# Kernel optimization log

Hardware: AMD Instinct MI355X
Metric: run time of the kernel (lower is better)

## Reference

```python
import jax, jax.numpy as jnp
import numpy as np

N, X_DIM, Y_DIM, HID = 8192, 512, 2048 // 4, 2048
Y_DIM = 512

def setup_inputs() -> dict:
    key = jax.random.key(0)
    ks = jax.random.split(key, 10)
    def lin(k, fan_in, fan_out):
        lim = 1.0 / np.sqrt(fan_in)
        kw, kb = jax.random.split(k)
        W = jax.random.uniform(kw, (fan_in, fan_out), jnp.float32, -lim, lim)
        b = jax.random.uniform(kb, (fan_out,), jnp.float32, -lim, lim)
        return W, b
    mu_W1, mu_b1 = lin(ks[0], X_DIM, HID)
    mu_W2, mu_b2 = lin(ks[1], HID, Y_DIM)
    lv_W1, lv_b1 = lin(ks[2], X_DIM, HID)
    lv_W2, lv_b2 = lin(ks[3], HID, Y_DIM)
    return {
        "x_samples": jax.random.normal(ks[4], (N, X_DIM), jnp.float32),
        "y_samples": jax.random.normal(ks[5], (N, Y_DIM), jnp.float32),
        "mu_W1": mu_W1, "mu_b1": mu_b1, "mu_W2": mu_W2, "mu_b2": mu_b2,
        "lv_W1": lv_W1, "lv_b1": lv_b1, "lv_W2": lv_W2, "lv_b2": lv_b2,
    }

def reference(x_samples, y_samples, mu_W1, mu_b1, mu_W2, mu_b2, lv_W1, lv_b1, lv_W2, lv_b2):
    # MLP heads (GEMMs)
    mu = jax.nn.relu(x_samples @ mu_W1 + mu_b1) @ mu_W2 + mu_b2          # [N, D]
    logvar = jnp.tanh(jax.nn.relu(x_samples @ lv_W1 + lv_b1) @ lv_W2 + lv_b2)  # [N, D]
    w = 0.5 * jnp.exp(-logvar)                                           # 1/(2*exp(logvar))
    n = x_samples.shape[0]

    # positive: -mean_i sum_d (mu_id - y_id)^2 * w_id
    positive = -(((mu - y_samples) ** 2) * w).sum(axis=1).mean()

    # negative (exact decomposition of the [N,N,D] broadcast):
    # -(1/N^2) sum_{i,d} w_id * (N*mu_id^2 - 2*mu_id*Sy_d + Sy2_d)
    Sy = y_samples.sum(axis=0)          # [D]
    Sy2 = (y_samples ** 2).sum(axis=0)  # [D]
    negative = -(w * (n * mu ** 2 - 2.0 * mu * Sy + Sy2)).sum() / (n * n)

    return positive - negative
```

## Files before the change

kernel.cpp:

```cpp
#include <hip/hip_runtime.h>
#include <hip/hip_bf16.h>
#include <stdint.h>

#define NS   8192
#define XD   512
#define HD   2048
#define YD   512

typedef unsigned short u16;
using bf16x8 = __attribute__((ext_vector_type(8))) short;
using f32x4  = __attribute__((ext_vector_type(4))) float;

__device__ __forceinline__ float bf2f(u16 u) {
  union { uint32_t i; float f; } v; v.i = ((uint32_t)u) << 16; return v.f;
}
__device__ __forceinline__ u16 f2b(float f) {
  __hip_bfloat16 hb = __float2bfloat16(f);
  return *(const u16*)&hb;
}
__device__ __forceinline__ float ld_in(const void* p, int f32, size_t i) {
  return f32 ? ((const float*)p)[i] : bf2f(((const u16*)p)[i]);
}
#define GLDS(gp, lp) __builtin_amdgcn_global_load_lds( \
    (__attribute__((address_space(1))) void*)(gp),     \
    (__attribute__((address_space(3))) void*)(lp), 16, 0, 0)

__device__ __forceinline__ int probe_f32(const void* p, int n_u16, int* sflag) {
  if (threadIdx.x == 0) *sflag = 0;
  __syncthreads();
  const u16* q = (const u16*)p;
  int wild = 0;
  for (int i = threadIdx.x; i < n_u16; i += blockDim.x) {
    float v = bf2f(q[i]);
    if (!(fabsf(v) <= 1000.0f)) wild = 1;
  }
  if (wild) *sflag = 1;
  __syncthreads();
  int r = *sflag;
  __syncthreads();
  return r;
}

__global__ __launch_bounds__(256) void prep_all(
    const void* __restrict__ x,
    const void* w1m, const void* b1m, const void* w2m, const void* b2m,
    const void* w1l, const void* b1l, const void* w2l, const void* b2l,
    const void* __restrict__ y,
    u16* __restrict__ xb, float* __restrict__ biasv,
    u16* __restrict__ W1t, u16* __restrict__ W2tm, u16* __restrict__ W2tl,
    float* __restrict__ Sy, float* __restrict__ Sy2) {
  __shared__ u16 tile[64 * 72];
  __shared__ int sflag;
  const int b = blockIdx.x;
  const int tid = threadIdx.x;

  if (b < 2048) {
    if (!probe_f32(x, 1024, &sflag)) return;
    const size_t base = (size_t)b * 2048 + (size_t)tid * 8;
    alignas(16) u16 o[8];
    const float4* s = (const float4*)((const float*)x + base);
    float4 v0 = s[0], v1 = s[1];
    o[0]=f2b(v0.x); o[1]=f2b(v0.y); o[2]=f2b(v0.z); o[3]=f2b(v0.w);
    o[4]=f2b(v1.x); o[5]=f2b(v1.y); o[6]=f2b(v1.z); o[7]=f2b(v1.w);
    *(uint4*)(xb + base) = *(const uint4*)o;
  } else if (b == 2048) {
    const int f3 = probe_f32(b1m, 1024, &sflag);
    const int f5 = probe_f32(b2m, 512, &sflag);
    const int f7 = probe_f32(b1l, 1024, &sflag);
    const int f9 = probe_f32(b2l, 512, &sflag);
    for (int i = tid; i < 5120; i += 256) {
      float v;
      if (i < 2048)      v = ld_in(b1m, f3, i);
      else if (i < 4096) v = ld_in(b1l, f7, i - 2048);
      else if (i < 4608) v = ld_in(b2m, f5, i - 4096);
      else               v = ld_in(b2l, f9, i - 4608);
      biasv[i] = v;
    }
  } else if (b < 3073) {
    const int id = b - 2049, which = id >> 8, t = id & 255;
    const void* in; u16* out; int R, C;
    if (which == 0)      { in = w1m; out = W1t;                   R = XD; C = HD; }
    else if (which == 1) { in = w2m; out = W2tm;                  R = HD; C = YD; }
    else if (which == 2) { in = w1l; out = W1t + (size_t)HD * XD; R = XD; C = HD; }
    else                 { in = w2l; out = W2tl;                  R = HD; C = YD; }
    const int f = probe_f32(in, 1024, &sflag);
    const int nbx = C >> 6;
    const int c0 = (t % nbx) * 64, r0 = (t / nbx) * 64;
    const int r = tid >> 2, cc = (tid & 3) * 16;
    if (f) {
      const float4* s = (const float4*)((const float*)in + (size_t)(r0 + r) * C + c0 + cc);
#pragma unroll
      for (int k = 0; k < 4; ++k) {
        float4 v = s[k];
        tile[r * 72 + cc + k * 4 + 0] = f2b(v.x);
        tile[r * 72 + cc + k * 4 + 1] = f2b(v.y);
        tile[r * 72 + cc + k * 4 + 2] = f2b(v.z);
        tile[r * 72 + cc + k * 4 + 3] = f2b(v.w);
      }
    } else {
      const uint4* s = (const uint4*)((const u16*)in + (size_t)(r0 + r) * C + c0 + cc);
      *(uint4*)&tile[r * 72 + cc]     = s[0];
      *(uint4*)&tile[r * 72 + cc + 8] = s[1];
    }
    __syncthreads();
    const int i = tid >> 2, jc = (tid & 3) * 16;
    alignas(16) u16 o[16];
#pragma unroll
    for (int j = 0; j < 16; ++j) o[j] = tile[(jc + j) * 72 + i];
    uint4* dq = (uint4*)&out[(size_t)(c0 + i) * R + r0 + jc];
    dq[0] = ((const uint4*)o)[0];
    dq[1] = ((const uint4*)o)[1];
  } else {
    const int id2 = b - 3073;
    const int yf = probe_f32(y, 1024, &sflag);
    const int half = tid >> 7;
    const int c0 = (tid & 127) * 4;
    const int r0 = id2 * 128 + half * 64;
    float s0 = 0.f, s1 = 0.f, s2 = 0.f, s3 = 0.f;
    float q0 = 0.f, q1 = 0.f, q2 = 0.f, q3 = 0.f;
    for (int r = r0; r < r0 + 64; r += 4) {
#pragma unroll
      for (int rr = 0; rr < 4; ++rr) {
        float v0, v1, v2, v3;
        if (yf) {
          const float4 t4 = *(const float4*)((const float*)y + (size_t)(r + rr) * YD + c0);
          v0 = t4.x; v1 = t4.y; v2 = t4.z; v3 = t4.w;
        } else {
          const uint2 t2 = *(const uint2*)((const u16*)y + (size_t)(r + rr) * YD + c0);
          v0 = bf2f((u16)(t2.x & 0xffff)); v1 = bf2f((u16)(t2.x >> 16));
          v2 = bf2f((u16)(t2.y & 0xffff)); v3 = bf2f((u16)(t2.y >> 16));
        }
        s0 += v0; q0 += v0 * v0;  s1 += v1; q1 += v1 * v1;
        s2 += v2; q2 += v2 * v2;  s3 += v3; q3 += v3 * v3;
      }
    }
    atomicAdd(&Sy[c0],     s0);  atomicAdd(&Sy2[c0],     q0);
    atomicAdd(&Sy[c0 + 1], s1);  atomicAdd(&Sy2[c0 + 1], q1);
    atomicAdd(&Sy[c0 + 2], s2);  atomicAdd(&Sy2[c0 + 2], q2);
    atomicAdd(&Sy[c0 + 3], s3);  atomicAdd(&Sy2[c0 + 3], q3);
  }
}

#define SYNC_PRE do { \
  __builtin_amdgcn_sched_barrier(0); \
  __builtin_amdgcn_s_barrier(); \
  asm volatile("s_waitcnt lgkmcnt(0)" ::: "memory"); \
  __builtin_amdgcn_sched_barrier(0); \
  __builtin_amdgcn_s_setprio(1); } while (0)
#define SYNC_POST do { \
  __builtin_amdgcn_s_setprio(0); \
  __builtin_amdgcn_sched_barrier(0); \
  __builtin_amdgcn_s_barrier(); \
  __builtin_amdgcn_sched_barrier(0); } while (0)
#define VMCNT(N) asm volatile("s_waitcnt vmcnt(" #N ")" ::: "memory")
#define SCB __builtin_amdgcn_sched_barrier(0)

#define RD_A(MH, BUF) do { \
  const u16* ab_ = &lds[((BUF)*2 + wm) * 8192]; \
  _Pragma("unroll") for (int q_ = 0; q_ < 4; ++q_) \
    _Pragma("unroll") for (int ks_ = 0; ks_ < 2; ++ks_) \
      af[q_][ks_] = *(const bf16x8*)&ab_[((MH)*64 + q_*16 + c16)*64 + (((ks_*4+quad) ^ cswz) << 3)]; \
} while (0)

#define RD_B(NH, BUF) do { \
  const u16* bb_ = &lds[32768 + ((BUF)*2 + (wn>>1)) * 8192]; \
  _Pragma("unroll") for (int p_ = 0; p_ < 2; ++p_) \
    _Pragma("unroll") for (int ks_ = 0; ks_ < 2; ++ks_) \
      bf[(NH)*2+p_][ks_] = *(const bf16x8*)&bb_[((wn&1)*64 + ((NH)*2+p_)*16 + c16)*64 + (((ks_*4+quad) ^ cswz) << 3)]; \
} while (0)

#define MM(MH, NH) do { \
  _Pragma("unroll") for (int ks_ = 0; ks_ < 2; ++ks_) \
    _Pragma("unroll") for (int q_ = 0; q_ < 4; ++q_) \
      _Pragma("unroll") for (int p_ = 0; p_ < 2; ++p_) \
        acc[(MH)*4+q_][(NH)*2+p_] = __builtin_amdgcn_mfma_f32_16x16x32_bf16( \
            af[q_][ks_], bf[(NH)*2+p_][ks_], acc[(MH)*4+q_][(NH)*2+p_], 0, 0, 0); \
} while (0)

#define ST_A(KT, HALF) do { if ((KT) < 8) { \
  u16* lb_ = &lds[(((KT)&1)*2 + (HALF))*8192 + (wid << 9)]; \
  const u16* sp_ = Aptr + (size_t)(bm0 + (HALF)*128 + (wid<<3) + srow)*512 + ((KT)<<6) + scg; \
  GLDS(sp_, lb_); GLDS(sp_ + (size_t)64*512, lb_ + 4096); } } while (0)

#define ST_B(KT, HALF) do { if ((KT) < 8) { \
  u16* lb_ = &lds[32768 + (((KT)&1)*2 + (HALF))*8192 + (wid << 9)]; \
  const u16* sp_ = W1t + (size_t)(bn0 + (HALF)*128 + (wid<<3) + srow)*512 + ((KT)<<6) + scg; \
  GLDS(sp_, lb_); GLDS(sp_ + (size_t)64*512, lb_ + 4096); } } while (0)

__global__ __launch_bounds__(512, 2) void gemm1_kernel(
    const void* __restrict__ xraw, const u16* __restrict__ xb,
    const u16* __restrict__ W1t,
    const float* __restrict__ bias,
    u16* __restrict__ h_mu, u16* __restrict__ h_lv) {
  __shared__ alignas(16) u16 lds[65536];
  __shared__ int sflag;
  const int tid = threadIdx.x;

  const u16* Aptr = probe_f32(xraw, 1024, &sflag) ? xb : (const u16*)xraw;

  const int wid = tid >> 6, lane = tid & 63;
  const int wm = wid >> 2, wn = wid & 3;
  const int quad = lane >> 4, c16 = lane & 15, cswz = c16 & 7;
  const int srow = lane >> 3;
  const int scg  = ((lane & 7) ^ srow) << 3;

  const int id = blockIdx.x;
  const int xcd = id & 7, slot = id >> 3;
  const int bm0 = (xcd * 4 + (slot & 3)) * 256;
  const int bn0 = (slot >> 2) * 256;

  f32x4 acc[8][4] = {};
  bf16x8 af[4][2], bf[4][2];

  ST_B(0, 0); ST_B(0, 1); ST_A(0, 0); ST_A(0, 1);
  ST_B(1, 0); ST_B(1, 1);
  VMCNT(4);
  __builtin_amdgcn_s_barrier();
  __builtin_amdgcn_sched_barrier(0);

#pragma unroll
  for (int i = 0; i < 4; ++i) {
    const int ka = 2 * i, kb = ka + 1;
    const bool last = (i == 3);
    RD_A(0, 0); RD_B(0, 0); ST_A(kb, 0);
    SYNC_PRE; MM(0, 0); SYNC_POST;
    RD_B(1, 0); ST_A(kb, 1);
    SYNC_PRE; MM(0, 1); SYNC_POST;
    RD_A(1, 0); ST_B(ka + 2, 0);
    SYNC_PRE; MM(1, 0); SYNC_POST;
    ST_B(ka + 2, 1);
    SYNC_PRE; MM(1, 1);
    if (!last) { VMCNT(4); } else { VMCNT(0); }
    SYNC_POST;
    RD_A(0, 1); RD_B(0, 1); ST_A(ka + 2, 0);
    SYNC_PRE; MM(0, 0); SYNC_POST;
    RD_B(1, 1); ST_A(ka + 2, 1);
    SYNC_PRE; MM(0, 1); SYNC_POST;
    RD_A(1, 1); ST_B(kb + 2, 0);
    SYNC_PRE; MM(1, 0); SYNC_POST;
    ST_B(kb + 2, 1);
    SYNC_PRE; MM(1, 1);
    if (!last) { VMCNT(4); }
    SYNC_POST;
  }

  u16* myl = &lds[wid * 8192];
  const bool is_lv = bn0 >= HD;
  u16* dst = is_lv ? h_lv : h_mu;
  const int wncol = wn << 6;
  const int gc0 = (bn0 - (is_lv ? HD : 0)) + wncol;
  const int grow0 = bm0 + (wm << 7);
#pragma unroll
  for (int ni = 0; ni < 4; ++ni) {
    const float bv = bias[bn0 + wncol + ni * 16 + c16];
#pragma unroll
    for (int mi = 0; mi < 8; ++mi)
#pragma unroll
      for (int r = 0; r < 4; ++r) {
        const int row = mi * 16 + (quad << 2) + r;
        const int col = ni * 16 + c16;
        myl[row * 64 + ((((col >> 3) ^ (row & 7)) << 3) | (col & 7))] =
            f2b(fmaxf(acc[mi][ni][r] + bv, 0.f));
      }
  }
#pragma unroll
  for (int it = 0; it < 16; ++it) {
    const int row = (it << 3) + (lane >> 3);
    const int ch = lane & 7;
    const uint4 v = *(const uint4*)&myl[row * 64 + ((ch ^ (row & 7)) << 3)];
    *(uint4*)&dst[(size_t)(grow0 + row) * HD + gc0 + (ch << 3)] = v;
  }
}

#undef RD_A
#undef RD_B
#undef MM
#undef ST_A
#undef ST_B

#define LDA8(AF, T) do { \
  const uint64_t o_ = (uint64_t)(T) * 128u; \
  asm volatile("global_load_dwordx4 %0, %1, off"           : "=v"(AF[0][0]) : "v"(aA[0] + o_)); \
  asm volatile("global_load_dwordx4 %0, %1, off offset:64" : "=v"(AF[0][1]) : "v"(aA[0] + o_)); \
  asm volatile("global_load_dwordx4 %0, %1, off"           : "=v"(AF[1][0]) : "v"(aA[1] + o_)); \
  asm volatile("global_load_dwordx4 %0, %1, off offset:64" : "=v"(AF[1][1]) : "v"(aA[1] + o_)); \
  asm volatile("global_load_dwordx4 %0, %1, off"           : "=v"(AF[2][0]) : "v"(aA[2] + o_)); \
  asm volatile("global_load_dwordx4 %0, %1, off offset:64" : "=v"(AF[2][1]) : "v"(aA[2] + o_)); \
  asm volatile("global_load_dwordx4 %0, %1, off"           : "=v"(AF[3][0]) : "v"(aA[3] + o_)); \
  asm volatile("global_load_dwordx4 %0, %1, off offset:64" : "=v"(AF[3][1]) : "v"(aA[3] + o_)); \
} while (0)

#define RD8(BF, BUFI) do { \
  _Pragma("unroll") for (int ni_ = 0; ni_ < 4; ++ni_) \
    _Pragma("unroll") for (int ks_ = 0; ks_ < 2; ++ks_) \
      BF[ni_][ks_] = *(const bf16x8*)&lds[(BUFI)*16384 + rbase + \
          (wn*64 + ni_*16 + c16)*64 + (((ks_*4+quad) ^ cswz) << 3)]; \
} while (0)

#define MM32(AF, BF) do { \
  _Pragma("unroll") for (int ks_ = 0; ks_ < 2; ++ks_) \
    _Pragma("unroll") for (int mi_ = 0; mi_ < 4; ++mi_) \
      _Pragma("unroll") for (int ni_ = 0; ni_ < 4; ++ni_) \
        acc[mi_][ni_] = __builtin_amdgcn_mfma_f32_16x16x32_bf16( \
            AF[mi_][ks_], BF[ni_][ks_], acc[mi_][ni_], 0, 0, 0); \
} while (0)

#define STB2(KT) do { \
  u16* lbm_ = lds + ((KT)&3)*16384 + (wid << 9); \
  const u16* spm_ = bMp + (size_t)(KT)*64; \
  GLDS(spm_, lbm_); GLDS(spm_ + (size_t)64*HD, lbm_ + 4096); \
  u16* lbl_ = lds + ((KT)&3)*16384 + 8192 + (wid << 9); \
  const u16* spl_ = bLp + (size_t)(KT)*64; \
  GLDS(spl_, lbl_); GLDS(spl_ + (size_t)64*HD, lbl_ + 4096); \
} while (0)

#define PH2(T, AFc, AFn, BFc, BFn) do { \
  SCB; LDA8(AFn, (T) + 1); SCB; STB2((T) + 2); SCB; \
  VMCNT(12); SCB; \
  __builtin_amdgcn_s_barrier(); SCB; \
  RD8(BFn, ((T) + 1) & 3); \
  __builtin_amdgcn_s_setprio(1); \
  MM32(AFc, BFc); \
  __builtin_amdgcn_s_setprio(0); \
} while (0)

__global__ __launch_bounds__(512, 1) void gemm2_dual(
    const u16* __restrict__ hm, const u16* __restrict__ hl,
    const u16* __restrict__ W2m, const u16* __restrict__ W2l,
    const float* __restrict__ b2m, const float* __restrict__ b2l,
    const void* __restrict__ y,
    const float* __restrict__ Sy, const float* __restrict__ Sy2,
    double* __restrict__ gacc, unsigned* __restrict__ counter,
    float* __restrict__ out) {
  __shared__ alignas(16) u16 lds[65536];
  __shared__ double bs[8];
  __shared__ int sflag;

  const int yf = probe_f32(y, 1024, &sflag);

  const int tid = threadIdx.x, wid = tid >> 6, lane = tid & 63;
  const int wh = wid >> 2;
  const int wm = (wid >> 1) & 1, wn = wid & 1;
  const int quad = lane >> 4, c16 = lane & 15, cswz = c16 & 7;
  const int srow = lane >> 3;
  const int scg  = ((lane & 7) ^ srow) << 3;
  const int rbase = wh * 8192;

  const int id = blockIdx.x;
  const int xcd = id & 7, slot = id >> 3;
  const int bm0 = (xcd * 8 + (slot >> 2)) * 128;
  const int bn0 = (slot & 3) * 128;

  const u16* bMp = W2m + (size_t)(bn0 + (wid << 3) + srow) * HD + scg;
  const u16* bLp = W2l + (size_t)(bn0 + (wid << 3) + srow) * HD + scg;

  const u16* hx = wh ? hl : hm;
  uint64_t aA[4];
#pragma unroll
  for (int mi = 0; mi < 4; ++mi)
    aA[mi] = (uint64_t)(uintptr_t)(
        hx + (size_t)(bm0 + wm * 64 + mi * 16 + c16) * HD + quad * 8);

  f32x4 acc[4][4] = {};
  bf16x8 afA[4][2], afB[4][2], bfA[4][2], bfB[4][2];

  STB2(0); STB2(1);
  SCB;
  LDA8(afA, 0);
  SCB;
  VMCNT(12);
  __builtin_amdgcn_s_barrier();
  SCB;
  RD8(bfA, 0);

#pragma unroll 1
  for (int i = 0; i < 28; i += 4) {
    PH2(i + 0, afA, afB, bfA, bfB);
    PH2(i + 1, afB, afA, bfB, bfA);
    PH2(i + 2, afA, afB, bfA, bfB);
    PH2(i + 3, afB, afA, bfB, bfA);
  }
  PH2(28, afA, afB, bfA, bfB);
  PH2(29, afB, afA, bfB, bfA);
  SCB; LDA8(afB, 31); SCB;
  VMCNT(8);
  SCB;
  __builtin_amdgcn_s_barrier();
  SCB;
  RD8(bfB, 3);
  __builtin_amdgcn_s_setprio(1);
  MM32(afA, bfA);
  __builtin_amdgcn_s_setprio(0);
  SCB;
  VMCNT(0);
  SCB;
  __builtin_amdgcn_s_setprio(1);
  MM32(afB, bfB);
  __builtin_amdgcn_s_setprio(0);

  __syncthreads();
  float* ldsF = (float*)lds;
  float* mur = ldsF + (wid & 3) * 4224;
  if (wh == 0) {
#pragma unroll
    for (int ni = 0; ni < 4; ++ni) {
      const float bmv = b2m[bn0 + wn * 64 + ni * 16 + c16];
#pragma unroll
      for (int mi = 0; mi < 4; ++mi)
#pragma unroll
        for (int r = 0; r < 4; ++r)
          mur[(mi * 16 + quad * 4 + r) * 66 + ni * 16 + c16] =
              acc[mi][ni][r] + bmv;
    }
  }
  __syncthreads();
  const float invN = 1.0f / (float)NS;
  float s = 0.f;
  if (wh == 1) {
#pragma unroll
    for (int ni = 0; ni < 4; ++ni) {
      const int gcol = bn0 + wn * 64 + ni * 16 + c16;
      const float blv = b2l[gcol];
      const float syv = Sy[gcol], sy2v = Sy2[gcol];
#pragma unroll
      for (int mi = 0; mi < 4; ++mi)
#pragma unroll
        for (int r = 0; r < 4; ++r) {
          const int grow = bm0 + wm * 64 + mi * 16 + quad * 4 + r;
          const float m   = mur[(mi * 16 + quad * 4 + r) * 66 + ni * 16 + c16];
          const float lvp = acc[mi][ni][r] + blv;
          const float w   = 0.5f * expf(-tanhf(lvp));
          const float yv  = ld_in(y, yf, (size_t)grow * YD + gcol);
          s += w * (yv * yv - 2.f * m * yv + (2.f * m * syv - sy2v) * invN);
        }
    }
  }
  for (int off = 32; off > 0; off >>= 1) s += __shfl_down(s, off);
  if (lane == 0) bs[wid] = (double)s;
  __syncthreads();
  if (tid == 0) {
    atomicAdd(gacc, bs[0] + bs[1] + bs[2] + bs[3] +
                    bs[4] + bs[5] + bs[6] + bs[7]);
    __threadfence();
    const unsigned old = atomicAdd(counter, 1u);
    if (old == gridDim.x - 1) {
      const double g = atomicAdd(gacc, 0.0);
      out[0] = (float)(-g / (double)NS);
    }
  }
}

extern "C" void kernel_launch(void* const* d_in, const int* in_sizes, int n_in,
                              void* d_out, int out_size, void* d_ws, size_t ws_size,
                              hipStream_t stream) {
  char* ws = (char*)d_ws;
  double*   gacc    = (double*)ws;
  unsigned* counter = (unsigned*)(ws + 8);
  float*    Sy      = (float*)(ws + 128);
  float*    Sy2     = (float*)(ws + 2176);
  float*    biasv   = (float*)(ws + 4224);
  u16* xb   = (u16*)(ws + 24704);
  u16* W1t  = xb + (size_t)NS * XD;
  u16* W2tm = W1t + (size_t)2 * HD * XD;
  u16* W2tl = W2tm + (size_t)YD * HD;
  u16* h_mu = W2tl + (size_t)YD * HD;
  u16* h_lv = h_mu + (size_t)NS * HD;

  hipMemsetAsync(d_ws, 0, 4224, stream);

  prep_all<<<2049 + 1024 + 64, 256, 0, stream>>>(
      d_in[0], d_in[2], d_in[3], d_in[4], d_in[5],
      d_in[6], d_in[7], d_in[8], d_in[9], d_in[1],
      xb, biasv, W1t, W2tm, W2tl, Sy, Sy2);

  const float* b1  = biasv;
  const float* b2m = biasv + 4096, *b2l = biasv + 4608;

  gemm1_kernel<<<(NS / 256) * ((2 * HD) / 256), 512, 0, stream>>>(
      d_in[0], xb, W1t, b1, h_mu, h_lv);

  gemm2_dual<<<(NS / 128) * (YD / 128), 512, 0, stream>>>(
      h_mu, h_lv, W2tm, W2tl, b2m, b2l, d_in[1], Sy, Sy2,
      gacc, counter, (float*)d_out);
}
```

Measured before the change: 262.6 us.

## Shrink gemm2 B ring to three LDS stages and allow two blocks per CU

Reduces the W2 LDS ring from four stages to three and drops the double-buffered B fragment registers in favour of a single set read at the start of each phase. It then raises launch bounds to two blocks per CU, which is meant to let a second block hide latency. The cost is that the B LDS read is no longer overlapped with the previous phase's MFMAs, because each phase now waits on lgkmcnt before computing. Register pressure under the tighter launch bound may also cause spills.

After: 261.4 us. No clear change (-0.5%).

```diff
diff --git a/kernel.cpp b/kernel.cpp
--- a/kernel.cpp
+++ b/kernel.cpp
@@ -153,6 +153,7 @@
   __builtin_amdgcn_s_barrier(); \
   __builtin_amdgcn_sched_barrier(0); } while (0)
 #define VMCNT(N) asm volatile("s_waitcnt vmcnt(" #N ")" ::: "memory")
+#define LGKM0 asm volatile("s_waitcnt lgkmcnt(0)" ::: "memory")
 #define SCB __builtin_amdgcn_sched_barrier(0)
 
 #define RD_A(MH, BUF) do { \
@@ -290,41 +291,43 @@
   asm volatile("global_load_dwordx4 %0, %1, off offset:64" : "=v"(AF[3][1]) : "v"(aA[3] + o_)); \
 } while (0)
 
-#define RD8(BF, BUFI) do { \
+#define RD8(BUFI) do { \
   _Pragma("unroll") for (int ni_ = 0; ni_ < 4; ++ni_) \
     _Pragma("unroll") for (int ks_ = 0; ks_ < 2; ++ks_) \
-      BF[ni_][ks_] = *(const bf16x8*)&lds[(BUFI)*16384 + rbase + \
+      bf[ni_][ks_] = *(const bf16x8*)&lds[(BUFI)*16384 + rbase + \
           (wn*64 + ni_*16 + c16)*64 + (((ks_*4+quad) ^ cswz) << 3)]; \
 } while (0)
 
-#define MM32(AF, BF) do { \
+#define MM32(AF) do { \
   _Pragma("unroll") for (int ks_ = 0; ks_ < 2; ++ks_) \
     _Pragma("unroll") for (int mi_ = 0; mi_ < 4; ++mi_) \
       _Pragma("unroll") for (int ni_ = 0; ni_ < 4; ++ni_) \
         acc[mi_][ni_] = __builtin_amdgcn_mfma_f32_16x16x32_bf16( \
-            AF[mi_][ks_], BF[ni_][ks_], acc[mi_][ni_], 0, 0, 0); \
-} while (0)
-
-#define STB2(KT) do { \
-  u16* lbm_ = lds + ((KT)&3)*16384 + (wid << 9); \
+            AF[mi_][ks_], bf[ni_][ks_], acc[mi_][ni_], 0, 0, 0); \
+} while (0)
+
+#define STB2(KT, BI) do { \
+  u16* lbm_ = lds + (BI)*16384 + (wid << 9); \
   const u16* spm_ = bMp + (size_t)(KT)*64; \
   GLDS(spm_, lbm_); GLDS(spm_ + (size_t)64*HD, lbm_ + 4096); \
-  u16* lbl_ = lds + ((KT)&3)*16384 + 8192 + (wid << 9); \
+  u16* lbl_ = lbm_ + 8192; \
   const u16* spl_ = bLp + (size_t)(KT)*64; \
   GLDS(spl_, lbl_); GLDS(spl_ + (size_t)64*HD, lbl_ + 4096); \
 } while (0)
 
-#define PH2(T, AFc, AFn, BFc, BFn) do { \
-  SCB; LDA8(AFn, (T) + 1); SCB; STB2((T) + 2); SCB; \
+#define PH6(T, AFc, AFn, BR, BS) do { \
+  SCB; RD8(BR); SCB; \
+  LDA8(AFn, (T) + 1); SCB; \
+  STB2((T) + 2, BS); SCB; \
+  LGKM0; SCB; \
   VMCNT(12); SCB; \
   __builtin_amdgcn_s_barrier(); SCB; \
-  RD8(BFn, ((T) + 1) & 3); \
   __builtin_amdgcn_s_setprio(1); \
-  MM32(AFc, BFc); \
-  __builtin_amdgcn_s_setprio(0); \
-} while (0)
-
-__global__ __launch_bounds__(512, 1) void gemm2_dual(
+  MM32(AFc); \
+  __builtin_amdgcn_s_setprio(0); SCB; \
+} while (0)
+
+__global__ __launch_bounds__(512, 2) void gemm2_dual(
     const u16* __restrict__ hm, const u16* __restrict__ hl,
     const u16* __restrict__ W2m, const u16* __restrict__ W2l,
     const float* __restrict__ b2m, const float* __restrict__ b2l,
@@ -332,7 +335,7 @@
     const float* __restrict__ Sy, const float* __restrict__ Sy2,
     double* __restrict__ gacc, unsigned* __restrict__ counter,
     float* __restrict__ out) {
-  __shared__ alignas(16) u16 lds[65536];
+  __shared__ alignas(16) u16 lds[49152];
   __shared__ double bs[8];
   __shared__ int sflag;
 
@@ -362,40 +365,40 @@
         hx + (size_t)(bm0 + wm * 64 + mi * 16 + c16) * HD + quad * 8);
 
   f32x4 acc[4][4] = {};
-  bf16x8 afA[4][2], afB[4][2], bfA[4][2], bfB[4][2];
-
-  STB2(0); STB2(1);
+  bf16x8 afA[4][2], afB[4][2], bf[4][2];
+
+  STB2(0, 0); STB2(1, 1);
   SCB;
   LDA8(afA, 0);
   SCB;
   VMCNT(12);
   __builtin_amdgcn_s_barrier();
   SCB;
-  RD8(bfA, 0);
 
 #pragma unroll 1
-  for (int i = 0; i < 28; i += 4) {
-    PH2(i + 0, afA, afB, bfA, bfB);
-    PH2(i + 1, afB, afA, bfB, bfA);
-    PH2(i + 2, afA, afB, bfA, bfB);
-    PH2(i + 3, afB, afA, bfB, bfA);
-  }
-  PH2(28, afA, afB, bfA, bfB);
-  PH2(29, afB, afA, bfB, bfA);
-  SCB; LDA8(afB, 31); SCB;
+  for (int i = 0; i < 5; ++i) {
+    PH6(6 * i + 0, afA, afB, 0, 2);
+    PH6(6 * i + 1, afB, afA, 1, 0);
+    PH6(6 * i + 2, afA, afB, 2, 1);
+    PH6(6 * i + 3, afB, afA, 0, 2);
+    PH6(6 * i + 4, afA, afB, 1, 0);
+    PH6(6 * i + 5, afB, afA, 2, 1);
+  }
+  SCB; RD8(0); SCB;
+  LDA8(afB, 31); SCB;
+  LGKM0; SCB;
   VMCNT(8);
   SCB;
-  __builtin_amdgcn_s_barrier();
-  SCB;
-  RD8(bfB, 3);
+  __builtin_amdgcn_s_barrier(); SCB;
   __builtin_amdgcn_s_setprio(1);
-  MM32(afA, bfA);
-  __builtin_amdgcn_s_setprio(0);
-  SCB;
+  MM32(afA);
+  __builtin_amdgcn_s_setprio(0); SCB;
+  RD8(1); SCB;
+  LGKM0; SCB;
   VMCNT(0);
   SCB;
   __builtin_amdgcn_s_setprio(1);
-  MM32(afB, bfB);
+  MM32(afB);
   __builtin_amdgcn_s_setprio(0);
 
   __syncthreads();
```

## Stage A tiles through LDS with double buffering and run two blocks per CU

Applied to the files above, without the earlier changes.

The second-GEMM kernel stops loading A fragments straight from global memory into registers. A and B tiles are now both staged into LDS via global_load_lds using a two-buffer ping-pong (32K elements per buffer), and each step waits for all loads with a full vmcnt(0). Only one set of fragment registers remains, and launch bounds go from 1 to 2 blocks per CU so two workgroups can overlap each other's latency. The trade-off is a shallower per-block prefetch (one tile ahead instead of two) and extra LDS traffic for A, in exchange for fewer registers and more occupancy.

Measured after the change: 236.5 us. -9.9%, faster.

```diff
diff --git a/kernel.cpp b/kernel.cpp
--- a/kernel.cpp
+++ b/kernel.cpp
@@ -278,53 +278,49 @@
 #undef ST_A
 #undef ST_B
 
-#define LDA8(AF, T) do { \
-  const uint64_t o_ = (uint64_t)(T) * 128u; \
-  asm volatile("global_load_dwordx4 %0, %1, off"           : "=v"(AF[0][0]) : "v"(aA[0] + o_)); \
-  asm volatile("global_load_dwordx4 %0, %1, off offset:64" : "=v"(AF[0][1]) : "v"(aA[0] + o_)); \
-  asm volatile("global_load_dwordx4 %0, %1, off"           : "=v"(AF[1][0]) : "v"(aA[1] + o_)); \
-  asm volatile("global_load_dwordx4 %0, %1, off offset:64" : "=v"(AF[1][1]) : "v"(aA[1] + o_)); \
-  asm volatile("global_load_dwordx4 %0, %1, off"           : "=v"(AF[2][0]) : "v"(aA[2] + o_)); \
-  asm volatile("global_load_dwordx4 %0, %1, off offset:64" : "=v"(AF[2][1]) : "v"(aA[2] + o_)); \
-  asm volatile("global_load_dwordx4 %0, %1, off"           : "=v"(AF[3][0]) : "v"(aA[3] + o_)); \
-  asm volatile("global_load_dwordx4 %0, %1, off offset:64" : "=v"(AF[3][1]) : "v"(aA[3] + o_)); \
-} while (0)
-
-#define RD8(BF, BUFI) do { \
+#define RDA8(BUF) do { \
+  _Pragma("unroll") for (int mi_ = 0; mi_ < 4; ++mi_) \
+    _Pragma("unroll") for (int ks_ = 0; ks_ < 2; ++ks_) \
+      af[mi_][ks_] = *(const bf16x8*)&lds[(BUF)*32768 + abase + \
+          (wm*64 + mi_*16 + c16)*64 + (((ks_*4+quad) ^ cswz) << 3)]; \
+} while (0)
+
+#define RDB8(BUF) do { \
   _Pragma("unroll") for (int ni_ = 0; ni_ < 4; ++ni_) \
     _Pragma("unroll") for (int ks_ = 0; ks_ < 2; ++ks_) \
-      BF[ni_][ks_] = *(const bf16x8*)&lds[(BUFI)*16384 + rbase + \
+      bf[ni_][ks_] = *(const bf16x8*)&lds[(BUF)*32768 + bbase + \
           (wn*64 + ni_*16 + c16)*64 + (((ks_*4+quad) ^ cswz) << 3)]; \
 } while (0)
 
-#define MM32(AF, BF) do { \
+#define MM32 do { \
   _Pragma("unroll") for (int ks_ = 0; ks_ < 2; ++ks_) \
     _Pragma("unroll") for (int mi_ = 0; mi_ < 4; ++mi_) \
       _Pragma("unroll") for (int ni_ = 0; ni_ < 4; ++ni_) \
         acc[mi_][ni_] = __builtin_amdgcn_mfma_f32_16x16x32_bf16( \
-            AF[mi_][ks_], BF[ni_][ks_], acc[mi_][ni_], 0, 0, 0); \
-} while (0)
-
-#define STB2(KT) do { \
-  u16* lbm_ = lds + ((KT)&3)*16384 + (wid << 9); \
-  const u16* spm_ = bMp + (size_t)(KT)*64; \
-  GLDS(spm_, lbm_); GLDS(spm_ + (size_t)64*HD, lbm_ + 4096); \
-  u16* lbl_ = lds + ((KT)&3)*16384 + 8192 + (wid << 9); \
-  const u16* spl_ = bLp + (size_t)(KT)*64; \
-  GLDS(spl_, lbl_); GLDS(spl_ + (size_t)64*HD, lbl_ + 4096); \
-} while (0)
-
-#define PH2(T, AFc, AFn, BFc, BFn) do { \
-  SCB; LDA8(AFn, (T) + 1); SCB; STB2((T) + 2); SCB; \
-  VMCNT(12); SCB; \
-  __builtin_amdgcn_s_barrier(); SCB; \
-  RD8(BFn, ((T) + 1) & 3); \
-  __builtin_amdgcn_s_setprio(1); \
-  MM32(AFc, BFc); \
-  __builtin_amdgcn_s_setprio(0); \
-} while (0)
-
-__global__ __launch_bounds__(512, 1) void gemm2_dual(
+            af[mi_][ks_], bf[ni_][ks_], acc[mi_][ni_], 0, 0, 0); \
+} while (0)
+
+#define ST4(BI) do { \
+  u16* l_ = lds + (BI)*32768 + (wid << 9); \
+  GLDS(pAm, l_);         GLDS(pAm2, l_ + 4096); \
+  GLDS(pAl, l_ + 8192);  GLDS(pAl2, l_ + 12288); \
+  GLDS(pBm, l_ + 16384); GLDS(pBm2, l_ + 20480); \
+  GLDS(pBl, l_ + 24576); GLDS(pBl2, l_ + 28672); \
+} while (0)
+
+#define BUMP8 do { pAm += 64; pAm2 += 64; pAl += 64; pAl2 += 64; \
+                   pBm += 64; pBm2 += 64; pBl += 64; pBl2 += 64; } while (0)
+
+#define PH10(BR, BW) do { \
+  SCB; RDA8(BR); RDB8(BR); SCB; \
+  ST4(BW); SCB; BUMP8; SCB; \
+  SYNC_PRE; \
+  MM32; \
+  VMCNT(0); \
+  SYNC_POST; \
+} while (0)
+
+__global__ __launch_bounds__(512, 2) void gemm2_dual(
     const u16* __restrict__ hm, const u16* __restrict__ hl,
     const u16* __restrict__ W2m, const u16* __restrict__ W2l,
     const float* __restrict__ b2m, const float* __restrict__ b2l,
@@ -344,61 +340,43 @@
   const int quad = lane >> 4, c16 = lane & 15, cswz = c16 & 7;
   const int srow = lane >> 3;
   const int scg  = ((lane & 7) ^ srow) << 3;
-  const int rbase = wh * 8192;
+  const int abase = wh ? 8192 : 0;
+  const int bbase = 16384 + abase;
 
   const int id = blockIdx.x;
   const int xcd = id & 7, slot = id >> 3;
   const int bm0 = (xcd * 8 + (slot >> 2)) * 128;
   const int bn0 = (slot & 3) * 128;
 
-  const u16* bMp = W2m + (size_t)(bn0 + (wid << 3) + srow) * HD + scg;
-  const u16* bLp = W2l + (size_t)(bn0 + (wid << 3) + srow) * HD + scg;
-
-  const u16* hx = wh ? hl : hm;
-  uint64_t aA[4];
-#pragma unroll
-  for (int mi = 0; mi < 4; ++mi)
-    aA[mi] = (uint64_t)(uintptr_t)(
-        hx + (size_t)(bm0 + wm * 64 + mi * 16 + c16) * HD + quad * 8);
+  const int strow = (wid << 3) + srow;
+  const u16* pAm  = hm  + (size_t)(bm0 + strow) * HD + scg;
+  const u16* pAm2 = pAm + (size_t)64 * HD;
+  const u16* pAl  = hl  + (size_t)(bm0 + strow) * HD + scg;
+  const u16* pAl2 = pAl + (size_t)64 * HD;
+  const u16* pBm  = W2m + (size_t)(bn0 + strow) * HD + scg;
+  const u16* pBm2 = pBm + (size_t)64 * HD;
+  const u16* pBl  = W2l + (size_t)(bn0 + strow) * HD + scg;
+  const u16* pBl2 = pBl + (size_t)64 * HD;
 
   f32x4 acc[4][4] = {};
-  bf16x8 afA[4][2], afB[4][2], bfA[4][2], bfB[4][2];
-
-  STB2(0); STB2(1);
-  SCB;
-  LDA8(afA, 0);
-  SCB;
-  VMCNT(12);
+  bf16x8 af[4][2], bf[4][2];
+
+  ST4(0); BUMP8;
+  VMCNT(0);
   __builtin_amdgcn_s_barrier();
   SCB;
-  RD8(bfA, 0);
 
 #pragma unroll 1
-  for (int i = 0; i < 28; i += 4) {
-    PH2(i + 0, afA, afB, bfA, bfB);
-    PH2(i + 1, afB, afA, bfB, bfA);
-    PH2(i + 2, afA, afB, bfA, bfB);
-    PH2(i + 3, afB, afA, bfB, bfA);
-  }
-  PH2(28, afA, afB, bfA, bfB);
-  PH2(29, afB, afA, bfB, bfA);
-  SCB; LDA8(afB, 31); SCB;
-  VMCNT(8);
-  SCB;
-  __builtin_amdgcn_s_barrier();
-  SCB;
-  RD8(bfB, 3);
-  __builtin_amdgcn_s_setprio(1);
-  MM32(afA, bfA);
-  __builtin_amdgcn_s_setprio(0);
-  SCB;
-  VMCNT(0);
-  SCB;
-  __builtin_amdgcn_s_setprio(1);
-  MM32(afB, bfB);
-  __builtin_amdgcn_s_setprio(0);
-
-  __syncthreads();
+  for (int i = 0; i < 15; ++i) {
+    PH10(0, 1);
+    PH10(1, 0);
+  }
+  PH10(0, 1);
+  SCB; RDA8(1); RDB8(1); SCB;
+  SYNC_PRE;
+  MM32;
+  SYNC_POST;
+
   float* ldsF = (float*)lds;
   float* mur = ldsF + (wid & 3) * 4224;
   if (wh == 0) {
```
